# Kernel tuning notes

Hardware: AMD Instinct MI355X
Metric: run time of the kernel (lower is better)

## Reference

```python
import jax, jax.numpy as jnp
import numpy as np

EPS = 1e-5

def setup_inputs() -> dict:
    key = jax.random.key(0)
    ks = jax.random.split(key, 4)
    B, C, H, W = 32, 256, 32, 32
    x = jax.random.normal(ks[0], (B, C, H, W), dtype=jnp.float32)
    gamma = jnp.ones((C,), dtype=jnp.float32)
    beta = jnp.zeros((C,), dtype=jnp.float32)
    # torch nn.Linear init scale ~ 1/sqrt(fan_in)
    W_kqv = jax.random.normal(ks[1], (3 * C, C), dtype=jnp.float32) / np.sqrt(C)
    b_kqv = jnp.zeros((3 * C,), dtype=jnp.float32)
    W_proj = jax.random.normal(ks[2], (C, C), dtype=jnp.float32) / np.sqrt(C)
    b_proj = jnp.zeros((C,), dtype=jnp.float32)
    return {"x": x, "gamma": gamma, "beta": beta, "W_kqv": W_kqv,
            "b_kqv": b_kqv, "W_proj": W_proj, "b_proj": b_proj}

def reference(x, gamma, beta, W_kqv, b_kqv, W_proj, b_proj):
    B, C, H, W = x.shape
    scale = jnp.sqrt(jnp.asarray(C, dtype=x.dtype))
    # BatchNorm2d (training-mode batch statistics, biased variance, eps=1e-5)
    mean = jnp.mean(x, axis=(0, 2, 3), keepdims=True)
    var = jnp.var(x, axis=(0, 2, 3), keepdims=True)
    t = (x - mean) * jax.lax.rsqrt(var + EPS)
    t = t * gamma[None, :, None, None] + beta[None, :, None, None]
    # [B, C, H, W] -> [B, N, C] with N = H*W
    t = t.reshape(B, C, H * W).transpose(0, 2, 1)
    kqv = t @ W_kqv.T + b_kqv           # [B, N, 3C]
    q, k, v = jnp.split(kqv, 3, axis=-1)  # each [B, N, C]
    s = jnp.einsum('bnc,bmc->bnm', q, k) / scale  # [B, N, N]
    attn = jax.nn.softmax(s, axis=-1)
    o = jnp.einsum('bnm,bmc->bnc', attn, v)        # [B, N, C]
    o = o @ W_proj.T + b_proj
    o = o.transpose(0, 2, 1).reshape(B, C, H, W)
    return o + x
```

## Files before the change

kernel.cpp:

```cpp
#include <hip/hip_runtime.h>

typedef unsigned short u16;
typedef __attribute__((ext_vector_type(8))) short bf16x8;
typedef __attribute__((ext_vector_type(4))) float f32x4;

__device__ __forceinline__ float bf2f(u16 u) {
  union { unsigned u; float f; } c; c.u = ((unsigned)u) << 16; return c.f;
}
__device__ __forceinline__ u16 f2bf(float f) {
  union { float f; unsigned u; } c; c.f = f;
  unsigned u = c.u;
  return (u16)((u + 0x7FFFu + ((u >> 16) & 1u)) >> 16);
}
__device__ __forceinline__ void gld16(const void* g, void* l) {
  __builtin_amdgcn_global_load_lds(
      (__attribute__((address_space(1))) void*)g,
      (__attribute__((address_space(3))) void*)l, 16, 0, 0);
}

#define SYNCB() do { \
  asm volatile("s_waitcnt vmcnt(0) lgkmcnt(0)" ::: "memory"); \
  __builtin_amdgcn_s_barrier(); \
  __builtin_amdgcn_sched_barrier(0); \
} while (0)

#define BB 32
#define CC 256
#define NN 1024

__global__ __launch_bounds__(256) void convert_w_kernel(
    const float* __restrict__ Wk, const float* __restrict__ bk,
    const float* __restrict__ Wp, const float* __restrict__ bp,
    u16* __restrict__ Wkb, u16* __restrict__ bkb,
    u16* __restrict__ Wpb, u16* __restrict__ bpb)
{
  int b = blockIdx.x, t = threadIdx.x;
  const float* src; u16* dst; int idx, n;
  if (b < 768)       { src = Wk; dst = Wkb; idx = b * 256 + t;        n = 196608; }
  else if (b < 771)  { src = bk; dst = bkb; idx = (b - 768) * 256 + t; n = 768;   }
  else if (b < 1027) { src = Wp; dst = Wpb; idx = (b - 771) * 256 + t; n = 65536; }
  else               { src = bp; dst = bpb; idx = t;                  n = 256;    }
  if (idx < n) dst[idx] = f2bf(src[idx]);
}

__global__ __launch_bounds__(256) void bn_stats_kernel(
    const float* __restrict__ x, const float* __restrict__ gamma,
    const float* __restrict__ beta, float* __restrict__ scl, float* __restrict__ sft)
{
  int c = blockIdx.x;
  int tid = threadIdx.x;
  float s = 0.f, q = 0.f;
  for (int g = tid; g < 8192; g += 256) {
    int b = g >> 8;
    int n = (g & 255) * 4;
    float4 v = *reinterpret_cast<const float4*>(x + (((size_t)(b * CC + c)) << 10) + n);
    s += v.x + v.y + v.z + v.w;
    q += v.x * v.x + v.y * v.y + v.z * v.z + v.w * v.w;
  }
  __shared__ float rs[256], rq[256];
  rs[tid] = s; rq[tid] = q;
  __syncthreads();
  for (int off = 128; off > 0; off >>= 1) {
    if (tid < off) { rs[tid] += rs[tid + off]; rq[tid] += rq[tid + off]; }
    __syncthreads();
  }
  if (tid == 0) {
    float mean = rs[0] * (1.f / 32768.f);
    float var  = rq[0] * (1.f / 32768.f) - mean * mean;
    float rstd = rsqrtf(var + 1e-5f);
    float g = gamma[c] * rstd;
    scl[c] = g;
    sft[c] = beta[c] - mean * g;
  }
}

__global__ __launch_bounds__(256) void norm_transpose_kernel(
    const float* __restrict__ x, const float* __restrict__ scl,
    const float* __restrict__ sft, u16* __restrict__ t)
{
  __shared__ float tile[64][65];
  int b = blockIdx.z, n0 = blockIdx.x * 64, c0 = blockIdx.y * 64;
  int tid = threadIdx.x;
  int hi = tid >> 4, lo4 = (tid & 15) * 4;
  #pragma unroll
  for (int r = 0; r < 4; ++r) {
    int cl = r * 16 + hi;
    int c = c0 + cl;
    float4 v = *reinterpret_cast<const float4*>(
        x + (((size_t)(b * CC + c)) << 10) + n0 + lo4);
    float sc = scl[c], sh = sft[c];
    tile[cl][lo4 + 0] = v.x * sc + sh;
    tile[cl][lo4 + 1] = v.y * sc + sh;
    tile[cl][lo4 + 2] = v.z * sc + sh;
    tile[cl][lo4 + 3] = v.w * sc + sh;
  }
  __syncthreads();
  #pragma unroll
  for (int r = 0; r < 4; ++r) {
    int nl = r * 16 + hi;
    ushort4 o;
    o.x = f2bf(tile[lo4 + 0][nl]);
    o.y = f2bf(tile[lo4 + 1][nl]);
    o.z = f2bf(tile[lo4 + 2][nl]);
    o.w = f2bf(tile[lo4 + 3][nl]);
    *reinterpret_cast<ushort4*>(t + ((size_t)(b * NN + n0 + nl)) * CC + c0 + lo4) = o;
  }
}

__global__ __launch_bounds__(256) void gemm_nt_kernel(
    const u16* __restrict__ A, int lda, size_t sA,
    const u16* __restrict__ B, int ldb, size_t sB,
    u16* __restrict__ C, int ldc, size_t sC,
    int K, const u16* __restrict__ bias, float scale, int mode,
    const float* __restrict__ xres, float* __restrict__ outf)
{
  __shared__ u16 As[128 * 32];
  __shared__ u16 Bs[128 * 32];
  int tid = threadIdx.x;
  int m0 = blockIdx.x * 128, n0 = blockIdx.y * 128;
  const u16* Ab = A + (size_t)blockIdx.z * sA;
  const u16* Bb = B + (size_t)blockIdx.z * sB;
  u16* Cb = C + (size_t)blockIdx.z * sC;

  int lane = tid & 63, w = tid >> 6;
  int lq = lane & 15, quad = lane >> 4;
  int wm = (w >> 1) * 64, wn = (w & 1) * 64;
  int ar = lane >> 2, ac = (lane & 3) * 8;
  int rb = w * 32;

  f32x4 zero = {0.f, 0.f, 0.f, 0.f};
  f32x4 acc[4][4];
  #pragma unroll
  for (int i = 0; i < 4; ++i)
    #pragma unroll
    for (int j = 0; j < 4; ++j) acc[i][j] = zero;

  for (int k0 = 0; k0 < K; k0 += 32) {
    __syncthreads();
    gld16(Ab + (size_t)(m0 + rb +      ar) * lda + k0 + ac, &As[(rb     ) * 32]);
    gld16(Ab + (size_t)(m0 + rb + 16 + ar) * lda + k0 + ac, &As[(rb + 16) * 32]);
    gld16(Bb + (size_t)(n0 + rb +      ar) * ldb + k0 + ac, &Bs[(rb     ) * 32]);
    gld16(Bb + (size_t)(n0 + rb + 16 + ar) * ldb + k0 + ac, &Bs[(rb + 16) * 32]);
    __syncthreads();
    bf16x8 af[4], bfr[4];
    #pragma unroll
    for (int i = 0; i < 4; ++i) {
      af[i]  = *reinterpret_cast<const bf16x8*>(&As[(wm + i * 16 + lq) * 32 + quad * 8]);
      bfr[i] = *reinterpret_cast<const bf16x8*>(&Bs[(wn + i * 16 + lq) * 32 + quad * 8]);
    }
    #pragma unroll
    for (int i = 0; i < 4; ++i)
      #pragma unroll
      for (int j = 0; j < 4; ++j)
        acc[i][j] = __builtin_amdgcn_mfma_f32_16x16x32_bf16(af[i], bfr[j], acc[i][j], 0, 0, 0);
  }

  #pragma unroll
  for (int j = 0; j < 4; ++j) {
    int col = n0 + wn + j * 16 + lq;
    float bv = bias ? bf2f(bias[col]) : 0.f;
    #pragma unroll
    for (int i = 0; i < 4; ++i) {
      int rbase = m0 + wm + i * 16 + quad * 4;
      if (mode == 2) {
        int b = rbase >> 10, n = rbase & 1023;
        size_t idx = (((size_t)(b * CC + col)) << 10) + n;
        float4 xv = *reinterpret_cast<const float4*>(xres + idx);
        float4 o;
        o.x = acc[i][j][0] * scale + bv + xv.x;
        o.y = acc[i][j][1] * scale + bv + xv.y;
        o.z = acc[i][j][2] * scale + bv + xv.z;
        o.w = acc[i][j][3] * scale + bv + xv.w;
        *reinterpret_cast<float4*>(outf + idx) = o;
      } else if (mode == 1) {
        int b = rbase >> 10, n = rbase & 1023;
        ushort4 o;
        o.x = f2bf(acc[i][j][0] * scale + bv);
        o.y = f2bf(acc[i][j][1] * scale + bv);
        o.z = f2bf(acc[i][j][2] * scale + bv);
        o.w = f2bf(acc[i][j][3] * scale + bv);
        *reinterpret_cast<ushort4*>(&Cb[(size_t)b * 262144 + (size_t)col * 1024 + n]) = o;
      } else {
        #pragma unroll
        for (int r = 0; r < 4; ++r)
          Cb[(size_t)(rbase + r) * ldc + col] = f2bf(acc[i][j][r] * scale + bv);
      }
    }
  }
}

__global__ __launch_bounds__(512, 2) void attn_kernel(
    const u16* __restrict__ qk,
    const u16* __restrict__ vt,
    u16* __restrict__ o)
{
  __shared__ __align__(16) u16 Ks[2][64 * 256];
  __shared__ __align__(16) u16 Vs[2][256 * 64];
  __shared__ __align__(16) u16 Ps[128 * 64];
  float* rs = (float*)Ps;

  int bid = blockIdx.x;
  int b  = (bid & 7) + 8 * ((bid >> 3) & 3);
  int qt = bid >> 5;
  int tid = threadIdx.x, lane = tid & 63, w = tid >> 6;
  int lq = lane & 15, hh = lane >> 4;
  int wr = w & 3;
  bool isQK = w < 4;

  const u16* qb = qk + ((size_t)b << 10) * 512;
  const u16* kb = qb + 256;
  const u16* vb = vt + ((size_t)b << 18);

  auto stageK = [&](int kt, int bufi) {
    #pragma unroll
    for (int i = 0; i < 4; ++i) {
      int slot = i * 512 + tid;
      int r = slot >> 5, c = slot & 31;
      gld16(kb + (size_t)(kt * 64 + r) * 512 + ((c ^ (r & 7)) << 3),
            &Ks[bufi][(i * 512 + (tid & 448)) * 8]);
    }
  };
  auto stageV = [&](int kt, int bufi) {
    #pragma unroll
    for (int i = 0; i < 4; ++i) {
      int slot = i * 512 + tid;
      int n = slot >> 3, c = slot & 7;
      gld16(vb + (size_t)(n << 10) + kt * 64 + ((c ^ (n & 7)) << 3),
            &Vs[bufi][(i * 512 + (tid & 448)) * 8]);
    }
  };

  f32x4 zero = {0.f, 0.f, 0.f, 0.f};

  stageK(0, 0);
  SYNCB();

  if (isQK) {
    int q0 = qt * 128 + wr * 32;
    bf16x8 qf[2][8];
    #pragma unroll
    for (int qi = 0; qi < 2; ++qi)
      #pragma unroll
      for (int kk = 0; kk < 8; ++kk)
        qf[qi][kk] = *reinterpret_cast<const bf16x8*>(
            qb + (size_t)(q0 + qi * 16 + lq) * 512 + kk * 32 + hh * 8);
    float runsum[2][4] = {{0.f, 0.f, 0.f, 0.f}, {0.f, 0.f, 0.f, 0.f}};

    #pragma unroll 1
    for (int p = 0; p <= 16; ++p) {
      if (p <= 15) stageV(p, p & 1);
      if (p <= 14) stageK(p + 1, (p + 1) & 1);
      u16 pbv[2][4][4];
      if (p <= 15) {
        const u16* Kc = Ks[p & 1];
        f32x4 sacc[2][4];
        #pragma unroll
        for (int qi = 0; qi < 2; ++qi)
          #pragma unroll
          for (int ni = 0; ni < 4; ++ni) sacc[qi][ni] = zero;
        #pragma unroll
        for (int kk = 0; kk < 8; ++kk) {
          bf16x8 kf[4];
          #pragma unroll
          for (int ni = 0; ni < 4; ++ni) {
            int r = ni * 16 + lq;
            kf[ni] = *reinterpret_cast<const bf16x8*>(
                &Kc[r * 256 + (((kk * 4 + hh) ^ (r & 7)) << 3)]);
          }
          __builtin_amdgcn_s_setprio(1);
          #pragma unroll
          for (int qi = 0; qi < 2; ++qi)
            #pragma unroll
            for (int ni = 0; ni < 4; ++ni)
              sacc[qi][ni] = __builtin_amdgcn_mfma_f32_16x16x32_bf16(
                  qf[qi][kk], kf[ni], sacc[qi][ni], 0, 0, 0);
          __builtin_amdgcn_s_setprio(0);
        }
        #pragma unroll
        for (int qi = 0; qi < 2; ++qi)
          #pragma unroll
          for (int ni = 0; ni < 4; ++ni)
            #pragma unroll
            for (int rr = 0; rr < 4; ++rr) {
              float pexp = __expf(sacc[qi][ni][rr] * 0.0625f);
              u16 pb = f2bf(pexp);
              runsum[qi][rr] += bf2f(pb);
              pbv[qi][ni][rr] = pb;
            }
      }
      SYNCB();
      if (p <= 15) {
        #pragma unroll
        for (int qi = 0; qi < 2; ++qi)
          #pragma unroll
          for (int ni = 0; ni < 4; ++ni)
            #pragma unroll
            for (int rr = 0; rr < 4; ++rr) {
              int q = wr * 32 + qi * 16 + hh * 4 + rr;
              int kcol = ni * 16 + lq;
              Ps[q * 64 + ((((kcol >> 3) ^ (q & 7)) << 3) | (kcol & 7))] =
                  pbv[qi][ni][rr];
            }
      }
      SYNCB();
    }

    #pragma unroll
    for (int qi = 0; qi < 2; ++qi)
      #pragma unroll
      for (int rr = 0; rr < 4; ++rr) {
        float s = runsum[qi][rr];
        s += __shfl_xor(s, 1, 64);
        s += __shfl_xor(s, 2, 64);
        s += __shfl_xor(s, 4, 64);
        s += __shfl_xor(s, 8, 64);
        if (lq == 0) rs[wr * 32 + qi * 16 + hh * 4 + rr] = 1.f / s;
      }
    SYNCB();
  } else {
    f32x4 oacc[8][4];
    #pragma unroll
    for (int qi = 0; qi < 8; ++qi)
      #pragma unroll
      for (int nj = 0; nj < 4; ++nj) oacc[qi][nj] = zero;

    #pragma unroll 1
    for (int p = 0; p <= 16; ++p) {
      if (p <= 15) stageV(p, p & 1);
      if (p <= 14) stageK(p + 1, (p + 1) & 1);
      if (p >= 1) {
        const u16* Vc = Vs[(p - 1) & 1];
        #pragma unroll
        for (int kk2 = 0; kk2 < 2; ++kk2) {
          bf16x8 pa[8];
          #pragma unroll
          for (int qi = 0; qi < 8; ++qi) {
            int r = qi * 16 + lq;
            pa[qi] = *reinterpret_cast<const bf16x8*>(
                &Ps[r * 64 + (((kk2 * 4 + hh) ^ (r & 7)) << 3)]);
          }
          bf16x8 vf[4];
          #pragma unroll
          for (int nj = 0; nj < 4; ++nj) {
            int n = wr * 64 + nj * 16 + lq;
            vf[nj] = *reinterpret_cast<const bf16x8*>(
                &Vc[n * 64 + (((kk2 * 4 + hh) ^ (n & 7)) << 3)]);
          }
          __builtin_amdgcn_s_setprio(1);
          #pragma unroll
          for (int qi = 0; qi < 8; ++qi)
            #pragma unroll
            for (int nj = 0; nj < 4; ++nj)
              oacc[qi][nj] = __builtin_amdgcn_mfma_f32_16x16x32_bf16(
                  pa[qi], vf[nj], oacc[qi][nj], 0, 0, 0);
          __builtin_amdgcn_s_setprio(0);
        }
      }
      SYNCB();
      SYNCB();
    }

    SYNCB();
    float rinv[8][4];
    #pragma unroll
    for (int qi = 0; qi < 8; ++qi)
      #pragma unroll
      for (int rr = 0; rr < 4; ++rr)
        rinv[qi][rr] = rs[qi * 16 + hh * 4 + rr];
    u16* ob = o + ((size_t)(b << 10) + qt * 128) * 256;
    #pragma unroll
    for (int qi = 0; qi < 8; ++qi)
      #pragma unroll
      for (int nj = 0; nj < 4; ++nj)
        #pragma unroll
        for (int rr = 0; rr < 4; ++rr)
          ob[(size_t)(qi * 16 + hh * 4 + rr) * 256 + wr * 64 + nj * 16 + lq] =
              f2bf(oacc[qi][nj][rr] * rinv[qi][rr]);
  }
}

extern "C" void kernel_launch(void* const* d_in, const int* in_sizes, int n_in,
                              void* d_out, int out_size, void* d_ws, size_t ws_size,
                              hipStream_t stream) {
  const float* x     = (const float*)d_in[0];
  const float* gamma = (const float*)d_in[1];
  const float* beta  = (const float*)d_in[2];
  const float* Wkqv  = (const float*)d_in[3];
  const float* bkqv  = (const float*)d_in[4];
  const float* Wproj = (const float*)d_in[5];
  const float* bproj = (const float*)d_in[6];
  float* out = (float*)d_out;

  char* ws = (char*)d_ws;
  float* scl    = (float*)ws;
  float* sft    = (float*)(ws + 1024);
  u16* Wkb = (u16*)(ws + 4096);
  u16* bkb = Wkb + 196608;
  u16* Wpb = bkb + 768;
  u16* bpb = Wpb + 65536;
  u16* qk   = (u16*)(ws + 1048576);
  u16* vt   = qk + (size_t)32768 * 512;
  u16* o_pv = vt + (size_t)32 * 256 * 1024;
  u16* t = (u16*)d_out;

  convert_w_kernel<<<dim3(1028), dim3(256), 0, stream>>>(
      Wkqv, bkqv, Wproj, bproj, Wkb, bkb, Wpb, bpb);
  bn_stats_kernel<<<dim3(256), dim3(256), 0, stream>>>(x, gamma, beta, scl, sft);
  norm_transpose_kernel<<<dim3(16, 4, 32), dim3(256), 0, stream>>>(x, scl, sft, t);
  gemm_nt_kernel<<<dim3(256, 4, 1), dim3(256), 0, stream>>>(
      t, 256, 0, Wkb, 256, 0, qk, 512, 0, 256, bkb, 1.0f, 0, nullptr, nullptr);
  gemm_nt_kernel<<<dim3(256, 2, 1), dim3(256), 0, stream>>>(
      t, 256, 0, Wkb + 512 * 256, 256, 0, vt, 0, 0, 256, bkb + 512, 1.0f, 1,
      nullptr, nullptr);
  attn_kernel<<<dim3(256), dim3(512), 0, stream>>>(qk, vt, o_pv);
  gemm_nt_kernel<<<dim3(256, 2, 1), dim3(256), 0, stream>>>(
      o_pv, 256, 0, Wpb, 256, 0, nullptr, 0, 0, 256, bpb, 1.0f, 2, x, out);
}
```

Baseline: 211.9 us.

## Fuse batchnorm-transpose into a single QKV projection GEMM kernel

Measured after the change: 203.8 us. -3.8%, faster.

```diff
diff --git a/kernel.cpp b/kernel.cpp
--- a/kernel.cpp
+++ b/kernel.cpp
@@ -74,36 +74,110 @@
   }
 }
 
-__global__ __launch_bounds__(256) void norm_transpose_kernel(
+__global__ __launch_bounds__(256, 2) void qkv_fused_kernel(
     const float* __restrict__ x, const float* __restrict__ scl,
-    const float* __restrict__ sft, u16* __restrict__ t)
+    const float* __restrict__ sft, const u16* __restrict__ Wkb,
+    const u16* __restrict__ bkb, u16* __restrict__ qkout, u16* __restrict__ vt)
 {
-  __shared__ float tile[64][65];
-  int b = blockIdx.z, n0 = blockIdx.x * 64, c0 = blockIdx.y * 64;
-  int tid = threadIdx.x;
-  int hi = tid >> 4, lo4 = (tid & 15) * 4;
+  __shared__ __align__(16) u16 As[128 * 32];
+  __shared__ __align__(16) u16 Bs[256 * 32];
+  int bid = blockIdx.x;
+  int bx = bid & 255, by = bid >> 8;
+  int b = bx >> 3, nsp0 = (bx & 7) * 128;
+  int tid = threadIdx.x, lane = tid & 63, w = tid >> 6;
+  int lq = lane & 15, quad = lane >> 4;
+  int wm = (w >> 1) * 64, wn = (w & 1) * 128;
+  int ar = lane >> 2, ac = (lane & 3) * 8;
+  int rbB = w * 64;
+  int nn = tid & 127, ci0 = (tid >> 7) * 16;
+
+  const float* xb = x + (((size_t)(b * CC)) << 10) + nsp0 + nn;
+  const u16* Bw = Wkb + (size_t)(by * 256) * 256;
+
+  f32x4 zero = {0.f, 0.f, 0.f, 0.f};
+  f32x4 acc[4][8];
   #pragma unroll
-  for (int r = 0; r < 4; ++r) {
-    int cl = r * 16 + hi;
-    int c = c0 + cl;
-    float4 v = *reinterpret_cast<const float4*>(
-        x + (((size_t)(b * CC + c)) << 10) + n0 + lo4);
-    float sc = scl[c], sh = sft[c];
-    tile[cl][lo4 + 0] = v.x * sc + sh;
-    tile[cl][lo4 + 1] = v.y * sc + sh;
-    tile[cl][lo4 + 2] = v.z * sc + sh;
-    tile[cl][lo4 + 3] = v.w * sc + sh;
-  }
-  __syncthreads();
-  #pragma unroll
-  for (int r = 0; r < 4; ++r) {
-    int nl = r * 16 + hi;
-    ushort4 o;
-    o.x = f2bf(tile[lo4 + 0][nl]);
-    o.y = f2bf(tile[lo4 + 1][nl]);
-    o.z = f2bf(tile[lo4 + 2][nl]);
-    o.w = f2bf(tile[lo4 + 3][nl]);
-    *reinterpret_cast<ushort4*>(t + ((size_t)(b * NN + n0 + nl)) * CC + c0 + lo4) = o;
+  for (int i = 0; i < 4; ++i)
+    #pragma unroll
+    for (int j = 0; j < 8; ++j) acc[i][j] = zero;
+
+  int swz = (nn >> 1) & 3;
+  int jj0 = ci0 >> 3;
+
+  for (int k0 = 0; k0 < 256; k0 += 32) {
+    __syncthreads();
+    #pragma unroll
+    for (int i = 0; i < 4; ++i)
+      gld16(Bw + (size_t)(rbB + i * 16 + ar) * 256 + k0 + ac,
+            &Bs[(rbB + i * 16) * 32]);
+    float sv[16], hv[16];
+    #pragma unroll
+    for (int g = 0; g < 4; ++g) {
+      float4 a = *reinterpret_cast<const float4*>(scl + k0 + ci0 + g * 4);
+      float4 d = *reinterpret_cast<const float4*>(sft + k0 + ci0 + g * 4);
+      sv[g * 4 + 0] = a.x; sv[g * 4 + 1] = a.y; sv[g * 4 + 2] = a.z; sv[g * 4 + 3] = a.w;
+      hv[g * 4 + 0] = d.x; hv[g * 4 + 1] = d.y; hv[g * 4 + 2] = d.z; hv[g * 4 + 3] = d.w;
+    }
+    u16 av[16];
+    #pragma unroll
+    for (int i = 0; i < 16; ++i) {
+      float v = xb[((size_t)(k0 + ci0 + i)) << 10];
+      av[i] = f2bf(v * sv[i] + hv[i]);
+    }
+    bf16x8 p0, p1;
+    #pragma unroll
+    for (int i = 0; i < 8; ++i) { p0[i] = (short)av[i]; p1[i] = (short)av[i + 8]; }
+    *reinterpret_cast<bf16x8*>(&As[nn * 32 + ((jj0 ^ swz) << 3)]) = p0;
+    *reinterpret_cast<bf16x8*>(&As[nn * 32 + (((jj0 + 1) ^ swz) << 3)]) = p1;
+    __syncthreads();
+
+    bf16x8 af[4], bfr[8];
+    #pragma unroll
+    for (int i = 0; i < 4; ++i) {
+      int r = wm + i * 16 + lq;
+      af[i] = *reinterpret_cast<const bf16x8*>(
+          &As[r * 32 + ((quad ^ ((r >> 1) & 3)) << 3)]);
+    }
+    #pragma unroll
+    for (int j = 0; j < 8; ++j)
+      bfr[j] = *reinterpret_cast<const bf16x8*>(
+          &Bs[(wn + j * 16 + lq) * 32 + quad * 8]);
+    #pragma unroll
+    for (int i = 0; i < 4; ++i)
+      #pragma unroll
+      for (int j = 0; j < 8; ++j)
+        acc[i][j] = __builtin_amdgcn_mfma_f32_16x16x32_bf16(af[i], bfr[j], acc[i][j], 0, 0, 0);
+  }
+
+  if (by < 2) {
+    #pragma unroll
+    for (int j = 0; j < 8; ++j) {
+      int col = by * 256 + wn + j * 16 + lq;
+      float bv = bf2f(bkb[col]);
+      #pragma unroll
+      for (int i = 0; i < 4; ++i) {
+        int m = (b << 10) + nsp0 + wm + i * 16 + quad * 4;
+        #pragma unroll
+        for (int r = 0; r < 4; ++r)
+          qkout[(size_t)(m + r) * 512 + col] = f2bf(acc[i][j][r] + bv);
+      }
+    }
+  } else {
+    #pragma unroll
+    for (int j = 0; j < 8; ++j) {
+      int col = wn + j * 16 + lq;
+      float bv = bf2f(bkb[512 + col]);
+      #pragma unroll
+      for (int i = 0; i < 4; ++i) {
+        int n = nsp0 + wm + i * 16 + quad * 4;
+        ushort4 o;
+        o.x = f2bf(acc[i][j][0] + bv);
+        o.y = f2bf(acc[i][j][1] + bv);
+        o.z = f2bf(acc[i][j][2] + bv);
+        o.w = f2bf(acc[i][j][3] + bv);
+        *reinterpret_cast<ushort4*>(&vt[(size_t)b * 262144 + (size_t)col * 1024 + n]) = o;
+      }
+    }
   }
 }
 
@@ -172,14 +246,6 @@
         o.z = acc[i][j][2] * scale + bv + xv.z;
         o.w = acc[i][j][3] * scale + bv + xv.w;
         *reinterpret_cast<float4*>(outf + idx) = o;
-      } else if (mode == 1) {
-        int b = rbase >> 10, n = rbase & 1023;
-        ushort4 o;
-        o.x = f2bf(acc[i][j][0] * scale + bv);
-        o.y = f2bf(acc[i][j][1] * scale + bv);
-        o.z = f2bf(acc[i][j][2] * scale + bv);
-        o.w = f2bf(acc[i][j][3] * scale + bv);
-        *reinterpret_cast<ushort4*>(&Cb[(size_t)b * 262144 + (size_t)col * 1024 + n]) = o;
       } else {
         #pragma unroll
         for (int r = 0; r < 4; ++r)
@@ -401,17 +467,12 @@
   u16* qk   = (u16*)(ws + 1048576);
   u16* vt   = qk + (size_t)32768 * 512;
   u16* o_pv = vt + (size_t)32 * 256 * 1024;
-  u16* t = (u16*)d_out;
 
   convert_w_kernel<<<dim3(1028), dim3(256), 0, stream>>>(
       Wkqv, bkqv, Wproj, bproj, Wkb, bkb, Wpb, bpb);
   bn_stats_kernel<<<dim3(256), dim3(256), 0, stream>>>(x, gamma, beta, scl, sft);
-  norm_transpose_kernel<<<dim3(16, 4, 32), dim3(256), 0, stream>>>(x, scl, sft, t);
-  gemm_nt_kernel<<<dim3(256, 4, 1), dim3(256), 0, stream>>>(
-      t, 256, 0, Wkb, 256, 0, qk, 512, 0, 256, bkb, 1.0f, 0, nullptr, nullptr);
-  gemm_nt_kernel<<<dim3(256, 2, 1), dim3(256), 0, stream>>>(
-      t, 256, 0, Wkb + 512 * 256, 256, 0, vt, 0, 0, 256, bkb + 512, 1.0f, 1,
-      nullptr, nullptr);
+  qkv_fused_kernel<<<dim3(768), dim3(256), 0, stream>>>(
+      x, scl, sft, Wkb, bkb, qk, vt);
   attn_kernel<<<dim3(256), dim3(512), 0, stream>>>(qk, vt, o_pv);
   gemm_nt_kernel<<<dim3(256, 2, 1), dim3(256), 0, stream>>>(
       o_pv, 256, 0, Wpb, 256, 0, nullptr, 0, 0, 256, bpb, 1.0f, 2, x, out);
```
